# Optimization experiments

Hardware: AMD Instinct MI355X
Metric: run time of the kernel (lower is better)

The kernel has to match this reference:

```python
import jax, jax.numpy as jnp
import numpy as np

K = 5       # local window size (odd)
G = 4       # groups

def _gconv1x1(x, w):
    # grouped 1x1 conv: x (b,c,h,w), w (g, c_out_g, c_in_g) -> (b,g,c_out_g,h,w)
    b, c, h, wd = x.shape
    g, co, ci = w.shape
    xg = x.reshape(b, g, ci, h, wd)
    return jnp.einsum('bgihw,goi->bgohw', xg, w)

def _windows(f, h, w):
    # f: (b,g,n,h+2p,w+2p) -> (b,g,n,h,w,K*K), row-major over (ki,kj)
    # matches torch .unfold(2,K,1).unfold(3,K,1).view(..., -1)
    return jnp.stack([f[..., i:i + h, j:j + w]
                      for i in range(K) for j in range(K)], axis=-1)

def setup_inputs() -> dict:
    key = jax.random.key(0)
    k1, k2, k3, k4 = jax.random.split(key, 4)
    x = jax.random.normal(k1, (2, 128, 96, 96), dtype=jnp.float32)
    wq = jax.random.normal(k2, (G, 32, 32), dtype=jnp.float32) * 0.1
    wk = jax.random.normal(k3, (G, 32, 32), dtype=jnp.float32) * 0.1
    wv = jax.random.normal(k4, (G, 32, 32), dtype=jnp.float32) * 0.1
    return {"x": x, "wq": wq, "wk": wk, "wv": wv}

def reference(x, wq, wk, wv):
    b, c, h, w = x.shape
    p = K // 2
    # query: plain grouped 1x1 conv, broadcast over window dim
    q = _gconv1x1(x, wq)[..., None]                      # (b,g,n,h,w,1)
    # key/value: reflect-pad (1x1 conv commutes with padding, same as torch's
    # Conv2d(..., padding=k//2, padding_mode='reflect'))
    xp = jnp.pad(x, ((0, 0), (0, 0), (p, p), (p, p)), mode='reflect')
    kf = _gconv1x1(xp, wk)                               # (b,g,n,h+2p,w+2p)
    vf = _gconv1x1(xp, wv)
    kwin = _windows(kf, h, w)                            # (b,g,n,h,w,K*K)
    vwin = _windows(vf, h, w)
    attn = jax.nn.softmax(q * kwin, axis=-1)             # per-channel window softmax
    y = (attn * vwin).sum(-1)                            # (b,g,n,h,w)
    return y.reshape(b, -1, h, w)                        # (b, c_out, h, w)
```

## Files before the change

### kernel.cpp

```cpp
#include <hip/hip_runtime.h>


#define HW 96
#define RG 12
#define NPOS 144

__device__ __forceinline__ int refl(int i) {
    i = (i < 0) ? -i : i;
    i = (i > 95) ? (190 - i) : i;
    return i;
}

__global__ __launch_bounds__(256) void fused_attn(
    const float* __restrict__ x, const float* __restrict__ wq,
    const float* __restrict__ wk, const float* __restrict__ wv,
    float* __restrict__ out)
{
    __shared__ float smem[4672 + 4608];
    float* const xs = smem;
    float* const kb = smem;
    float* const vb = smem + 4672;

    const int tid  = threadIdx.x;
    const int tile = blockIdx.x;
    const int g    = blockIdx.y;
    const int b    = blockIdx.z;
    const int h0 = (tile / 12) * 8;
    const int w0 = (tile % 12) * 8;

    const float* xg = x + (size_t)(b * 128 + g * 32) * (HW * HW);

    for (int idx = tid; idx < 32 * NPOS; idx += 256) {
        int pos = idx % NPOS;
        int ch  = idx / NPOS;
        int iy = refl(h0 + pos / RG - 2);
        int ix = refl(w0 + pos % RG - 2);
        xs[idx] = xg[ch * (HW * HW) + iy * HW + ix];
    }
    __syncthreads();

    const int wid  = tid >> 6;
    const int lane = tid & 63;
    const int n0   = __builtin_amdgcn_readfirstlane(wid * 8);
    const float* wkp = wk + (g * 32 + n0) * 32;
    const float* wvp = wv + (g * 32 + n0) * 32;
    const float* wqp = wq + (g * 32 + n0) * 32;

    const int ty = lane >> 3, tx = lane & 7;
    const int center = (ty + 2) * RG + (tx + 2);

    float qacc[8];
    float ak0[8], ak1[8], ak2[8], av0[8], av1[8], av2[8];
    #pragma unroll
    for (int n = 0; n < 8; n++) {
        qacc[n] = 0.f;
        ak0[n]=ak1[n]=ak2[n]=0.f; av0[n]=av1[n]=av2[n]=0.f;
    }
    #pragma unroll 4
    for (int i = 0; i < 32; i++) {
        float xq = xs[i * NPOS + center];
        float x0 = xs[i * NPOS + lane];
        float x1 = xs[i * NPOS + 64 + lane];
        float x2 = xs[i * NPOS + 128 + lane];
        #pragma unroll
        for (int n = 0; n < 8; n++) {
            float a = wkp[n * 32 + i];
            float c = wvp[n * 32 + i];
            qacc[n] += wqp[n * 32 + i] * xq;
            ak0[n] += a * x0; ak1[n] += a * x1; ak2[n] += a * x2;
            av0[n] += c * x0; av1[n] += c * x1; av2[n] += c * x2;
        }
    }
    __syncthreads();

    #pragma unroll
    for (int n = 0; n < 8; n++) {
        kb[(n0 + n) * NPOS + lane]      = ak0[n];
        vb[(n0 + n) * NPOS + lane]      = av0[n];
        kb[(n0 + n) * NPOS + 64 + lane] = ak1[n];
        vb[(n0 + n) * NPOS + 64 + lane] = av1[n];
        if (lane < 16) {
            kb[(n0 + n) * NPOS + 128 + lane] = ak2[n];
            vb[(n0 + n) * NPOS + 128 + lane] = av2[n];
        }
    }
    __syncthreads();

    float* outp = out + (size_t)((b * 128 + g * 32 + n0) * HW + (h0 + ty)) * HW + (w0 + tx);
    for (int n = 0; n < 8; n++) {
        const float* kbn = kb + (n0 + n) * NPOS;
        const float* vbn = vb + (n0 + n) * NPOS;
        float q = qacc[n];
        float den = 0.f, num = 0.f;
        #pragma unroll
        for (int t = 0; t < 25; t++) {
            int dy = t / 5, dx = t % 5;
            float e = __expf(q * kbn[(ty + dy) * RG + tx + dx]);
            den += e;
            num += e * vbn[(ty + dy) * RG + tx + dx];
        }
        outp[n * (HW * HW)] = num * __builtin_amdgcn_rcpf(den);
    }
}

extern "C" void kernel_launch(void* const* d_in, const int* in_sizes, int n_in,
                              void* d_out, int out_size, void* d_ws, size_t ws_size,
                              hipStream_t stream) {
    const float* x  = (const float*)d_in[0];
    const float* wq = (const float*)d_in[1];
    const float* wk = (const float*)d_in[2];
    const float* wv = (const float*)d_in[3];
    float* out = (float*)d_out;

    dim3 grid(144, 4, 2);
    fused_attn<<<grid, 256, 0, stream>>>(x, wq, wk, wv, out);
}
```

Before: 104.0 us.

## Compute grouped 1x1 projections with bf16 MFMA and pack K/V in shared memory

Replaces the scalar FP32 FMA loops for the q/k/v grouped 1x1 convolutions with bf16 16x16x32 MFMA instructions. Inputs and weights are converted to bf16, x is stored channel-interleaved, and k/v are packed as bf16 pairs into one 32-bit shared word with a padded stride, which shrinks LDS use and halves LDS reads in the softmax loop. It also uses exp2 with a pre-scaled q and requests higher occupancy through launch bounds. The trade-off is lower precision in q, k, v and the exponent, which may exceed tolerance.

```diff
diff --git a/kernel.cpp b/kernel.cpp
--- a/kernel.cpp
+++ b/kernel.cpp
@@ -1,9 +1,14 @@
 #include <hip/hip_runtime.h>
+#include <hip/hip_bf16.h>
 
 
 #define HW 96
 #define RG 12
 #define NPOS 144
+#define KVSTR 145
+
+typedef short short8 __attribute__((ext_vector_type(8)));
+typedef float float4v __attribute__((ext_vector_type(4)));
 
 __device__ __forceinline__ int refl(int i) {
     i = (i < 0) ? -i : i;
@@ -11,93 +16,115 @@
     return i;
 }
 
-__global__ __launch_bounds__(256) void fused_attn(
+__device__ __forceinline__ unsigned short f2bf(float f) {
+    __hip_bfloat16 h = __float2bfloat16(f);
+    return *reinterpret_cast<unsigned short*>(&h);
+}
+__device__ __forceinline__ float bfbits2f(unsigned int lo16) {
+    return __uint_as_float(lo16 << 16);
+}
+
+__global__ __launch_bounds__(256, 5) void fused_attn(
     const float* __restrict__ x, const float* __restrict__ wq,
     const float* __restrict__ wk, const float* __restrict__ wv,
     float* __restrict__ out)
 {
-    __shared__ float smem[4672 + 4608];
-    float* const xs = smem;
-    float* const kb = smem;
-    float* const vb = smem + 4672;
+    __shared__ unsigned short xs[NPOS * 32];
+    __shared__ unsigned int   kvb[32 * KVSTR];
+    __shared__ unsigned short qs[32 * 64];
 
-    const int tid  = threadIdx.x;
-    const int tile = blockIdx.x;
-    const int g    = blockIdx.y;
-    const int b    = blockIdx.z;
-    const int h0 = (tile / 12) * 8;
-    const int w0 = (tile % 12) * 8;
-
+    const int tid = threadIdx.x;
+    const int g = blockIdx.y, b = blockIdx.z;
+    const int h0 = (blockIdx.x / 12) * 8;
+    const int w0 = (blockIdx.x % 12) * 8;
     const float* xg = x + (size_t)(b * 128 + g * 32) * (HW * HW);
 
-    for (int idx = tid; idx < 32 * NPOS; idx += 256) {
-        int pos = idx % NPOS;
-        int ch  = idx / NPOS;
+    #pragma unroll
+    for (int it = 0; it < 9; it++) {
+        int idx = it * 256 + tid;
+        int cp  = idx / NPOS;
+        int pos = idx - cp * NPOS;
         int iy = refl(h0 + pos / RG - 2);
         int ix = refl(w0 + pos % RG - 2);
-        xs[idx] = xg[ch * (HW * HW) + iy * HW + ix];
+        const float* p = xg + (2 * cp) * (HW * HW) + iy * HW + ix;
+        float a = p[0], c = p[HW * HW];
+        unsigned int pk = (unsigned int)f2bf(a) | ((unsigned int)f2bf(c) << 16);
+        *(unsigned int*)&xs[pos * 32 + 2 * cp] = pk;
     }
-    __syncthreads();
 
     const int wid  = tid >> 6;
     const int lane = tid & 63;
-    const int n0   = __builtin_amdgcn_readfirstlane(wid * 8);
-    const float* wkp = wk + (g * 32 + n0) * 32;
-    const float* wvp = wv + (g * 32 + n0) * 32;
-    const float* wqp = wq + (g * 32 + n0) * 32;
+    const int n0   = wid * 8;
+    const int col  = lane & 15;
+    const int quad = lane >> 4;
+    const int koff = quad * 8;
 
-    const int ty = lane >> 3, tx = lane & 7;
-    const int center = (ty + 2) * RG + (tx + 2);
+    const float* wrow = (col < 8) ? (wk + (g * 32 + n0 + col) * 32)
+                                  : (wv + (g * 32 + n0 + col - 8) * 32);
+    short8 bkv;
+    #pragma unroll
+    for (int j = 0; j < 8; j++)
+        ((unsigned short*)&bkv)[j] = f2bf(wrow[koff + j]);
 
-    float qacc[8];
-    float ak0[8], ak1[8], ak2[8], av0[8], av1[8], av2[8];
-    #pragma unroll
-    for (int n = 0; n < 8; n++) {
-        qacc[n] = 0.f;
-        ak0[n]=ak1[n]=ak2[n]=0.f; av0[n]=av1[n]=av2[n]=0.f;
+    short8 bq = {0, 0, 0, 0, 0, 0, 0, 0};
+    if (col < 8) {
+        const float* qr = wq + (g * 32 + n0 + col) * 32;
+        #pragma unroll
+        for (int j = 0; j < 8; j++)
+            ((unsigned short*)&bq)[j] = f2bf(qr[koff + j]);
     }
-    #pragma unroll 4
-    for (int i = 0; i < 32; i++) {
-        float xq = xs[i * NPOS + center];
-        float x0 = xs[i * NPOS + lane];
-        float x1 = xs[i * NPOS + 64 + lane];
-        float x2 = xs[i * NPOS + 128 + lane];
-        #pragma unroll
-        for (int n = 0; n < 8; n++) {
-            float a = wkp[n * 32 + i];
-            float c = wvp[n * 32 + i];
-            qacc[n] += wqp[n * 32 + i] * xq;
-            ak0[n] += a * x0; ak1[n] += a * x1; ak2[n] += a * x2;
-            av0[n] += c * x0; av1[n] += c * x1; av2[n] += c * x2;
-        }
-    }
+
     __syncthreads();
 
     #pragma unroll
-    for (int n = 0; n < 8; n++) {
-        kb[(n0 + n) * NPOS + lane]      = ak0[n];
-        vb[(n0 + n) * NPOS + lane]      = av0[n];
-        kb[(n0 + n) * NPOS + 64 + lane] = ak1[n];
-        vb[(n0 + n) * NPOS + 64 + lane] = av1[n];
-        if (lane < 16) {
-            kb[(n0 + n) * NPOS + 128 + lane] = ak2[n];
-            vb[(n0 + n) * NPOS + 128 + lane] = av2[n];
+    for (int t = 0; t < 9; t++) {
+        int p = t * 16 + col;
+        short8 a = *(const short8*)&xs[p * 32 + koff];
+        float4v d = {0.f, 0.f, 0.f, 0.f};
+        d = __builtin_amdgcn_mfma_f32_16x16x32_bf16(a, bkv, d, 0, 0, 0);
+        int c = n0 + (col & 7);
+        unsigned short* dst0 = (unsigned short*)&kvb[c * KVSTR + t * 16 + quad * 4];
+        int half = (col < 8) ? 0 : 1;
+        #pragma unroll
+        for (int r = 0; r < 4; r++)
+            dst0[2 * r + half] = f2bf(d[r]);
+    }
+
+    #pragma unroll
+    for (int t = 0; t < 4; t++) {
+        int mp = t * 16 + col;
+        int p  = ((mp >> 3) + 2) * RG + (mp & 7) + 2;
+        short8 a = *(const short8*)&xs[p * 32 + koff];
+        float4v d = {0.f, 0.f, 0.f, 0.f};
+        d = __builtin_amdgcn_mfma_f32_16x16x32_bf16(a, bq, d, 0, 0, 0);
+        if (col < 8) {
+            unsigned int* dst = (unsigned int*)&qs[(n0 + col) * 64 + t * 16 + quad * 4];
+            dst[0] = (unsigned int)f2bf(d[0]) | ((unsigned int)f2bf(d[1]) << 16);
+            dst[1] = (unsigned int)f2bf(d[2]) | ((unsigned int)f2bf(d[3]) << 16);
         }
     }
+
     __syncthreads();
 
+    const int ty = lane >> 3, tx = lane & 7;
     float* outp = out + (size_t)((b * 128 + g * 32 + n0) * HW + (h0 + ty)) * HW + (w0 + tx);
     for (int n = 0; n < 8; n++) {
-        const float* kbn = kb + (n0 + n) * NPOS;
-        const float* vbn = vb + (n0 + n) * NPOS;
-        float q = qacc[n];
+        int c = n0 + n;
+        float q = bfbits2f(qs[c * 64 + lane]) * 1.44269504f;
         float den = 0.f, num = 0.f;
         #pragma unroll
-        for (int t = 0; t < 25; t++) {
-            int dy = t / 5, dx = t % 5;
-            float e = __expf(q * kbn[(ty + dy) * RG + tx + dx]);
-            den += e;
-            num += e * vbn[(ty + dy) * RG + tx + dx];
+        for (int dy = 0; dy < 5; dy++) {
+            const unsigned int* rowp = &kvb[c * KVSTR + (ty + dy) * RG + tx];
+            #pragma unroll
+            for (int dx = 0; dx < 5; dx++) {
+                unsigned int u = rowp[dx];
+                float kf = __uint_as_float(u << 16);
+                float vf = __uint_as_float(u & 0xffff0000u);
+                float e;
+                asm("v_exp_f32 %0, %1" : "=v"(e) : "v"(q * kf));
+                den += e;
+                num = fmaf(e, vf, num);
+            }
         }
         outp[n * (HW * HW)] = num * __builtin_amdgcn_rcpf(den);
     }
```

Result: faster. 92.73 us (-10.9%).
